# Optimization experiments

Measured on AMD Instinct MI355X. Metric: run time of the kernel, lower is better.

The kernel has to match this reference:

```python
import jax, jax.numpy as jnp
import numpy as np

N_NODES = 50000
N_EDGES = 800000
D = 64  # in_dim = hidden = out_dim
LEAKY_SLOPE = 0.01  # F.leaky_relu default


def gat_layer(h, src, dst, W, b, aW, ab):
    # fc: z = h @ W.T + b            [N, D_out]
    z = h @ W.T + b
    zs = z[src]                       # gather src feats  [E, D_out]
    zd = z[dst]                       # gather dst feats  [E, D_out]
    # attn_fc(concat(z_src, z_dst)) -> scalar per edge, then leaky_relu
    e = jnp.concatenate([zs, zd], axis=-1) @ aW.T + ab   # [E, 1]
    e = jax.nn.leaky_relu(e, LEAKY_SLOPE)[:, 0]          # [E]
    # softmax over incoming edges per destination node (mailbox softmax)
    m = jax.ops.segment_max(e, dst, num_segments=N_NODES)    # [N]
    ex = jnp.exp(e - m[dst])
    den = jax.ops.segment_sum(ex, dst, num_segments=N_NODES)  # [N]
    alpha = ex / den[dst]                                      # [E]
    # scatter-sum aggregate of alpha * z_src
    return jax.ops.segment_sum(alpha[:, None] * zs, dst, num_segments=N_NODES)


def setup_inputs() -> dict:
    key = jax.random.key(0)
    ks = jax.random.split(key, 16)
    x = jax.random.normal(ks[0], (N_NODES, D), dtype=jnp.float32)
    src = jax.random.randint(ks[1], (N_EDGES,), 0, N_NODES)
    dst = jax.random.randint(ks[2], (N_EDGES,), 0, N_NODES)
    # xavier_normal with relu gain, per reset_parameters
    gain = float(np.sqrt(2.0))
    params = {}
    for i in range(3):
        std_fc = gain * np.sqrt(2.0 / (D + D))
        std_at = gain * np.sqrt(2.0 / (2 * D + 1))
        params[f"W{i}"] = jax.random.normal(ks[3 + 4 * i], (D, D), dtype=jnp.float32) * std_fc
        params[f"b{i}"] = jnp.zeros((D,), dtype=jnp.float32)
        params[f"a{i}"] = jax.random.normal(ks[4 + 4 * i], (1, 2 * D), dtype=jnp.float32) * std_at
        params[f"ab{i}"] = jnp.zeros((1,), dtype=jnp.float32)
    return {"x": x, "src": src, "dst": dst, **params}


def reference(x, src, dst, W0, b0, a0, ab0, W1, b1, a1, ab1, W2, b2, a2, ab2):
    h = gat_layer(x, src, dst, W0, b0, a0, ab0)
    h = jax.nn.relu(h)
    h = gat_layer(h, src, dst, W1, b1, a1, ab1)
    h = jax.nn.relu(h)
    h = gat_layer(h, src, dst, W2, b2, a2, ab2)
    return h
```

## Files before the change

### kernel.cpp

```cpp
#include <hip/hip_runtime.h>
#include <math.h>

#define N_NODES 50000
#define N_EDGES 800000
#define D 64

#define NB 256
#define NBLK 256
#define BUCKET_NODES 196
#define TILE 3125

typedef unsigned short ushort_t;

__device__ __forceinline__ ushort_t f32_to_bf16(float f) {
    unsigned u = __float_as_uint(f);
    u += 0x7fffu + ((u >> 16) & 1u);
    return (ushort_t)(u >> 16);
}

template<int N>
__global__ void scan_partial_g(const int* __restrict__ in, int* __restrict__ partials) {
    const int base = blockIdx.x * 1024 + threadIdx.x * 4;
    int4 c = make_int4(0, 0, 0, 0);
    if (base + 3 < N) c = *(const int4*)&in[base];
    else { int* cp = (int*)&c; for (int j = 0; j < 4; ++j) if (base + j < N) cp[j] = in[base + j]; }
    int s = c.x + c.y + c.z + c.w;
    #pragma unroll
    for (int off = 32; off >= 1; off >>= 1) s += __shfl_xor(s, off, 64);
    __shared__ int red[4];
    if ((threadIdx.x & 63) == 0) red[threadIdx.x >> 6] = s;
    __syncthreads();
    if (threadIdx.x == 0) partials[blockIdx.x] = red[0] + red[1] + red[2] + red[3];
}

template<int N, int NT>
__global__ void scan_write_i(const int* __restrict__ in, const int* __restrict__ partials_raw,
                             int* __restrict__ out) {
    __shared__ int toff;
    __shared__ int sh[256];
    const int tid = threadIdx.x;
    if (tid < 64) {
        const int v = (tid < NT) ? partials_raw[tid] : 0;
        int inc = v;
        #pragma unroll
        for (int off = 1; off < 64; off <<= 1) {
            const int w = __shfl_up(inc, off, 64);
            if (tid >= off) inc += w;
        }
        if (tid == blockIdx.x) toff = inc - v;
    }
    const int base = blockIdx.x * 1024 + tid * 4;
    int4 c = make_int4(0, 0, 0, 0);
    if (base + 3 < N) c = *(const int4*)&in[base];
    else { int* cp = (int*)&c; for (int j = 0; j < 4; ++j) if (base + j < N) cp[j] = in[base + j]; }
    const int s = c.x + c.y + c.z + c.w;
    sh[tid] = s;
    __syncthreads();
    for (int off = 1; off < 256; off <<= 1) {
        const int w = (tid >= off) ? sh[tid - off] : 0;
        __syncthreads();
        sh[tid] += w;
        __syncthreads();
    }
    int run = toff + sh[tid] - s;
    const int* cp = (const int*)&c;
    int rp[4];
    #pragma unroll
    for (int j = 0; j < 4; ++j) { rp[j] = run; run += cp[j]; }
    if (base + 3 < N) *(int4*)&out[base] = make_int4(rp[0], rp[1], rp[2], rp[3]);
    else for (int j = 0; j < 4; ++j) if (base + j < N) out[base + j] = rp[j];
}

__global__ __launch_bounds__(256) void bucket_hist(const int* __restrict__ dst,
                                                   int* __restrict__ Acnt) {
    __shared__ int hist[NB];
    for (int i = threadIdx.x; i < NB; i += 256) hist[i] = 0;
    __syncthreads();
    const int base = blockIdx.x * TILE;
    for (int i = threadIdx.x; i < TILE; i += 256)
        atomicAdd(&hist[dst[base + i] / BUCKET_NODES], 1);
    __syncthreads();
    for (int bk = threadIdx.x; bk < NB; bk += 256)
        Acnt[bk * NBLK + blockIdx.x] = hist[bk];
}

__global__ __launch_bounds__(256) void bucket_scatter(const int* __restrict__ src,
                                                      const int* __restrict__ dst,
                                                      const int* __restrict__ offs,
                                                      int2* __restrict__ staging) {
    __shared__ int cur[NB];
    for (int i = threadIdx.x; i < NB; i += 256) cur[i] = offs[i * NBLK + blockIdx.x];
    __syncthreads();
    const int base = blockIdx.x * TILE;
    for (int i = threadIdx.x; i < TILE; i += 256) {
        const int s = src[base + i], d = dst[base + i];
        const int pos = atomicAdd(&cur[d / BUCKET_NODES], 1);
        staging[pos] = make_int2(s, d);
    }
}

__global__ __launch_bounds__(256) void node_counts(const int2* __restrict__ staging,
                                                   const int* __restrict__ offs,
                                                   int* __restrict__ counts,
                                                   int* __restrict__ bucket_sum) {
    __shared__ int cnt[BUCKET_NODES];
    __shared__ int red[4];
    const int b = blockIdx.x, tid = threadIdx.x;
    for (int i = tid; i < BUCKET_NODES; i += 256) cnt[i] = 0;
    __syncthreads();
    const int s0 = offs[b * NBLK];
    const int s1 = (b == NB - 1) ? N_EDGES : offs[(b + 1) * NBLK];
    for (int i = s0 + tid; i < s1; i += 256)
        atomicAdd(&cnt[staging[i].y - b * BUCKET_NODES], 1);
    __syncthreads();
    for (int i = tid; i < BUCKET_NODES; i += 256) {
        const int node = b * BUCKET_NODES + i;
        if (node < N_NODES) counts[node] = cnt[i];
    }
    int s = (tid < BUCKET_NODES) ? cnt[tid] : 0;
    #pragma unroll
    for (int off = 32; off >= 1; off >>= 1) s += __shfl_xor(s, off, 64);
    if ((tid & 63) == 0) red[tid >> 6] = s;
    __syncthreads();
    if (tid == 0) bucket_sum[b] = red[0] + red[1] + red[2] + red[3];
}

__global__ __launch_bounds__(256) void row_ptr_build(const int* __restrict__ counts,
                                                     const int* __restrict__ bucket_sum,
                                                     int* __restrict__ row_ptr) {
    __shared__ int bs[NB];
    __shared__ int loc[256];
    const int b = blockIdx.x, tid = threadIdx.x;
    bs[tid] = bucket_sum[tid];
    __syncthreads();
    for (int off = 1; off < 256; off <<= 1) {
        const int w = (tid >= off) ? bs[tid - off] : 0;
        __syncthreads();
        bs[tid] += w;
        __syncthreads();
    }
    const int bucket_off = bs[b] - bucket_sum[b];
    const int node = b * BUCKET_NODES + tid;
    const int c = (tid < BUCKET_NODES && node < N_NODES) ? counts[node] : 0;
    loc[tid] = c;
    __syncthreads();
    for (int off = 1; off < 256; off <<= 1) {
        const int w = (tid >= off) ? loc[tid - off] : 0;
        __syncthreads();
        loc[tid] += w;
        __syncthreads();
    }
    if (tid < BUCKET_NODES && node < N_NODES) row_ptr[node] = bucket_off + loc[tid] - c;
    if (b == 0 && tid == 0) row_ptr[N_NODES] = N_EDGES;
}

__global__ __launch_bounds__(256) void bucket_to_csr(const int2* __restrict__ staging,
                                                     const int* __restrict__ offs,
                                                     const int* __restrict__ row_ptr,
                                                     int* __restrict__ csr_src) {
    __shared__ int cur[BUCKET_NODES];
    const int b = blockIdx.x;
    for (int i = threadIdx.x; i < BUCKET_NODES; i += 256) {
        const int node = b * BUCKET_NODES + i;
        cur[i] = (node < N_NODES) ? row_ptr[node] : 0;
    }
    __syncthreads();
    const int s0 = offs[b * NBLK];
    const int s1 = (b == NB - 1) ? N_EDGES : offs[(b + 1) * NBLK];
    for (int i = s0 + threadIdx.x; i < s1; i += 256) {
        const int2 e = staging[i];
        const int pos = atomicAdd(&cur[e.y - b * BUCKET_NODES], 1);
        csr_src[pos] = e.x;
    }
}

#define NL_ROWS 8
__global__ __launch_bounds__(256) void node_linear_gemm(
    const float* __restrict__ h, ushort_t* __restrict__ zb,
    const float* __restrict__ W, const float* __restrict__ b,
    const float* __restrict__ a, const float* __restrict__ ab,
    float* __restrict__ s_src, float* __restrict__ s_dst)
{
    __shared__ float Wt[64 * 65];
    for (int idx = threadIdx.x; idx < D * D; idx += 256) {
        const int j = idx >> 6, k = idx & 63;
        Wt[k * 65 + j] = W[idx];
    }
    __syncthreads();

    const int lane = threadIdx.x & 63;
    const int wv   = __builtin_amdgcn_readfirstlane(threadIdx.x >> 6);
    const int row0 = (blockIdx.x * 4 + wv) * NL_ROWS;
    if (row0 >= N_NODES) return;

    const float bj  = b[lane];
    const float alo = a[lane];
    const float ahi = a[64 + lane];

    const float* hr[NL_ROWS];
    #pragma unroll
    for (int r = 0; r < NL_ROWS; ++r) hr[r] = h + (size_t)(row0 + r) * D;

    float acc[NL_ROWS];
    #pragma unroll
    for (int r = 0; r < NL_ROWS; ++r) acc[r] = bj;

    #pragma unroll 4
    for (int k = 0; k < D; ++k) {
        const float wkj = Wt[k * 65 + lane];
        #pragma unroll
        for (int r = 0; r < NL_ROWS; ++r)
            acc[r] = fmaf(hr[r][k], wkj, acc[r]);
    }

    #pragma unroll
    for (int r = 0; r < NL_ROWS; ++r) {
        zb[(size_t)(row0 + r) * D + lane] = f32_to_bf16(acc[r]);
        float u = acc[r] * alo;
        float v = acc[r] * ahi;
        #pragma unroll
        for (int off = 32; off >= 1; off >>= 1) {
            u += __shfl_xor(u, off, 64);
            v += __shfl_xor(v, off, 64);
        }
        if (lane == 0) { s_src[row0 + r] = u; s_dst[row0 + r] = v + ab[0]; }
    }
}

template<bool RELU>
__global__ __launch_bounds__(256) void fused_softmax_gather(
    const int* __restrict__ row_ptr, const int* __restrict__ csr_src,
    const float* __restrict__ s_src, const float* __restrict__ s_dst,
    const ushort_t* __restrict__ zb, float* __restrict__ out)
{
    __shared__ int2 sh[4][64];
    const int lane = threadIdx.x & 63;
    const int wv   = threadIdx.x >> 6;
    const int g    = lane >> 4;
    const int sl   = lane & 15;
    const int node0 = (blockIdx.x * 4 + wv) * 4;
    if (node0 >= N_NODES) return;
    const int mynode = node0 + g;

    const int beg = row_ptr[mynode];
    const int end = row_ptr[mynode + 1];
    const float sd = s_dst[mynode];
    float m = -INFINITY, den = 0.f;
    for (int base = beg; base < end; base += 16) {
        const int n = min(16, end - base);
        float e = -INFINITY;
        if (sl < n) {
            const int s = csr_src[base + sl];
            e = s_src[s] + sd;
            e = e > 0.f ? e : 0.01f * e;
        }
        float mc = e;
        #pragma unroll
        for (int off = 8; off >= 1; off >>= 1) mc = fmaxf(mc, __shfl_xor(mc, off, 64));
        if (mc > m) { den *= __expf(m - mc); m = mc; }
        float ex = (sl < n) ? __expf(e - m) : 0.f;
        #pragma unroll
        for (int off = 8; off >= 1; off >>= 1) ex += __shfl_xor(ex, off, 64);
        den += ex;
    }
    const float invden = (den > 0.f) ? 1.f / den : 0.f;

    const int half = lane >> 5;
    const int fl   = lane & 31;
    #pragma unroll
    for (int q = 0; q < 4; ++q) {
        const int nq    = node0 + q;
        const int begq  = __shfl(beg, q * 16, 64);
        const int endq  = __shfl(end, q * 16, 64);
        const float mq  = __shfl(m, q * 16, 64);
        const float ivq = __shfl(invden, q * 16, 64);
        const float sdq = __shfl(sd, q * 16, 64);

        float2 acc[8];
        #pragma unroll
        for (int p = 0; p < 8; ++p) acc[p] = make_float2(0.f, 0.f);

        for (int base = begq; base < endq; base += 64) {
            const int n = min(64, endq - base);
            int2 ws = make_int2(0, 0);
            if (lane < n) {
                const int s = csr_src[base + lane];
                float e = s_src[s] + sdq;
                e = e > 0.f ? e : 0.01f * e;
                ws = make_int2(__float_as_int(__expf(e - mq) * ivq), s);
            }
            sh[wv][lane] = ws;
            for (int t = 0; t < n; t += 16) {
                #pragma unroll
                for (int p = 0; p < 8; ++p) {
                    const int ei = t + 2 * p + half;
                    const int2 w2 = sh[wv][ei];
                    const float w = __int_as_float(w2.x);
                    const unsigned u = *(const unsigned*)&zb[(size_t)w2.y * D + 2 * fl];
                    acc[p].x = fmaf(w, __uint_as_float(u << 16), acc[p].x);
                    acc[p].y = fmaf(w, __uint_as_float(u & 0xffff0000u), acc[p].y);
                }
            }
        }
        float2 tot = make_float2(0.f, 0.f);
        #pragma unroll
        for (int p = 0; p < 8; ++p) { tot.x += acc[p].x; tot.y += acc[p].y; }
        tot.x += __shfl_xor(tot.x, 32, 64);
        tot.y += __shfl_xor(tot.y, 32, 64);
        if (RELU) { tot.x = fmaxf(tot.x, 0.f); tot.y = fmaxf(tot.y, 0.f); }
        if (half == 0)
            *(float2*)&out[(size_t)nq * D + 2 * fl] = tot;
    }
}

extern "C" void kernel_launch(void* const* d_in, const int* in_sizes, int n_in,
                              void* d_out, int out_size, void* d_ws, size_t ws_size,
                              hipStream_t stream) {
    const float* x   = (const float*)d_in[0];
    const int*   src = (const int*)d_in[1];
    const int*   dst = (const int*)d_in[2];
    float* out = (float*)d_out;

    char* wp = (char*)d_ws;
    auto alloc = [&](size_t bytes) -> void* {
        void* p = (void*)wp;
        wp += (bytes + 255) & ~(size_t)255;
        return p;
    };
    ushort_t* zb      = (ushort_t*)alloc((size_t)N_NODES * D * sizeof(ushort_t));
    float* s_src      = (float*)alloc((size_t)N_NODES * sizeof(float));
    float* s_dst      = (float*)alloc((size_t)N_NODES * sizeof(float));
    int*   counts     = (int*)alloc((size_t)N_NODES * sizeof(int));
    int*   row_ptr    = (int*)alloc((size_t)(N_NODES + 1) * sizeof(int));
    int*   csr_src    = (int*)alloc((size_t)N_EDGES * sizeof(int));
    int*   partB      = (int*)alloc(64 * sizeof(int));
    int*   bucket_sum = (int*)alloc((size_t)NB * sizeof(int));
    int*   Acnt       = (int*)alloc((size_t)NB * NBLK * sizeof(int));
    int*   offs       = (int*)alloc((size_t)NB * NBLK * sizeof(int));
    int2*  staging    = (int2*)alloc((size_t)N_EDGES * sizeof(int2));
    (void)ws_size;

    bucket_hist<<<NBLK, 256, 0, stream>>>(dst, Acnt);
    scan_partial_g<NB * NBLK><<<64, 256, 0, stream>>>(Acnt, partB);
    scan_write_i<NB * NBLK, 64><<<64, 256, 0, stream>>>(Acnt, partB, offs);
    bucket_scatter<<<NBLK, 256, 0, stream>>>(src, dst, offs, staging);
    node_counts<<<NB, 256, 0, stream>>>(staging, offs, counts, bucket_sum);
    row_ptr_build<<<NB, 256, 0, stream>>>(counts, bucket_sum, row_ptr);
    bucket_to_csr<<<NB, 256, 0, stream>>>(staging, offs, row_ptr, csr_src);

    const int grid_k1 = (N_NODES + 4 * NL_ROWS - 1) / (4 * NL_ROWS);
    const int grid_fg = N_NODES / 16;

    for (int layer = 0; layer < 3; ++layer) {
        const float* W  = (const float*)d_in[3 + 4 * layer];
        const float* b  = (const float*)d_in[4 + 4 * layer];
        const float* a  = (const float*)d_in[5 + 4 * layer];
        const float* ab = (const float*)d_in[6 + 4 * layer];
        const float* hin = (layer == 0) ? x : out;

        node_linear_gemm<<<grid_k1, 256, 0, stream>>>(hin, zb, W, b, a, ab, s_src, s_dst);
        if (layer < 2) {
            fused_softmax_gather<true ><<<grid_fg, 256, 0, stream>>>(row_ptr, csr_src, s_src, s_dst, zb, out);
        } else {
            fused_softmax_gather<false><<<grid_fg, 256, 0, stream>>>(row_ptr, csr_src, s_src, s_dst, zb, out);
        }
    }
}
```

Baseline: 199.6 us.

## Interleave gather of four destination nodes per wave in one edge loop

The aggregation phase now handles the four nodes owned by a wave together instead of one after another. Edge weights for all four nodes are staged in shared memory, then a single loop walks up to the largest degree and issues gathers for all four nodes in each step. The aim is more independent memory loads in flight and fewer serialized short loops. The cost is padded work: the loop runs to the maximum of the four degrees, and zero-weighted rows get loaded where a node has fewer edges.

```diff
diff --git a/kernel.cpp b/kernel.cpp
--- a/kernel.cpp
+++ b/kernel.cpp
@@ -233,7 +233,7 @@
     const float* __restrict__ s_src, const float* __restrict__ s_dst,
     const ushort_t* __restrict__ zb, float* __restrict__ out)
 {
-    __shared__ int2 sh[4][64];
+    __shared__ int2 sh[4][4][64];
     const int lane = threadIdx.x & 63;
     const int wv   = threadIdx.x >> 6;
     const int g    = lane >> 4;
@@ -265,51 +265,68 @@
     }
     const float invden = (den > 0.f) ? 1.f / den : 0.f;
 
+    int begq[4], endq[4];
+    float mq[4], ivq[4], sdq[4];
+    #pragma unroll
+    for (int q = 0; q < 4; ++q) {
+        begq[q] = __shfl(beg, q * 16, 64);
+        endq[q] = __shfl(end, q * 16, 64);
+        mq[q]   = __shfl(m, q * 16, 64);
+        ivq[q]  = __shfl(invden, q * 16, 64);
+        sdq[q]  = __shfl(sd, q * 16, 64);
+    }
+    int maxdeg = 0;
+    #pragma unroll
+    for (int q = 0; q < 4; ++q) maxdeg = max(maxdeg, endq[q] - begq[q]);
+
     const int half = lane >> 5;
     const int fl   = lane & 31;
+    float2 acc[4][2];
     #pragma unroll
     for (int q = 0; q < 4; ++q) {
-        const int nq    = node0 + q;
-        const int begq  = __shfl(beg, q * 16, 64);
-        const int endq  = __shfl(end, q * 16, 64);
-        const float mq  = __shfl(m, q * 16, 64);
-        const float ivq = __shfl(invden, q * 16, 64);
-        const float sdq = __shfl(sd, q * 16, 64);
-
-        float2 acc[8];
-        #pragma unroll
-        for (int p = 0; p < 8; ++p) acc[p] = make_float2(0.f, 0.f);
-
-        for (int base = begq; base < endq; base += 64) {
-            const int n = min(64, endq - base);
+        acc[q][0] = make_float2(0.f, 0.f);
+        acc[q][1] = make_float2(0.f, 0.f);
+    }
+
+    for (int c = 0; c < maxdeg; c += 64) {
+        #pragma unroll
+        for (int q = 0; q < 4; ++q) {
             int2 ws = make_int2(0, 0);
-            if (lane < n) {
-                const int s = csr_src[base + lane];
-                float e = s_src[s] + sdq;
+            const int i = begq[q] + c + lane;
+            if (i < endq[q]) {
+                const int s = csr_src[i];
+                float e = s_src[s] + sdq[q];
                 e = e > 0.f ? e : 0.01f * e;
-                ws = make_int2(__float_as_int(__expf(e - mq) * ivq), s);
+                ws = make_int2(__float_as_int(__expf(e - mq[q]) * ivq[q]), s);
             }
-            sh[wv][lane] = ws;
-            for (int t = 0; t < n; t += 16) {
-                #pragma unroll
-                for (int p = 0; p < 8; ++p) {
-                    const int ei = t + 2 * p + half;
-                    const int2 w2 = sh[wv][ei];
-                    const float w = __int_as_float(w2.x);
-                    const unsigned u = *(const unsigned*)&zb[(size_t)w2.y * D + 2 * fl];
-                    acc[p].x = fmaf(w, __uint_as_float(u << 16), acc[p].x);
-                    acc[p].y = fmaf(w, __uint_as_float(u & 0xffff0000u), acc[p].y);
-                }
+            sh[wv][q][lane] = ws;
+        }
+        const int n = min(64, maxdeg - c);
+        for (int t = 0; t < n; t += 4) {
+            #pragma unroll
+            for (int q = 0; q < 4; ++q) {
+                const int2 wa = sh[wv][q][t + half];
+                const int2 wb = sh[wv][q][t + 2 + half];
+                const unsigned ua = *(const unsigned*)&zb[(size_t)wa.y * D + 2 * fl];
+                const unsigned ub = *(const unsigned*)&zb[(size_t)wb.y * D + 2 * fl];
+                const float fa = __int_as_float(wa.x);
+                const float fb = __int_as_float(wb.x);
+                acc[q][0].x = fmaf(fa, __uint_as_float(ua << 16), acc[q][0].x);
+                acc[q][0].y = fmaf(fa, __uint_as_float(ua & 0xffff0000u), acc[q][0].y);
+                acc[q][1].x = fmaf(fb, __uint_as_float(ub << 16), acc[q][1].x);
+                acc[q][1].y = fmaf(fb, __uint_as_float(ub & 0xffff0000u), acc[q][1].y);
             }
         }
-        float2 tot = make_float2(0.f, 0.f);
-        #pragma unroll
-        for (int p = 0; p < 8; ++p) { tot.x += acc[p].x; tot.y += acc[p].y; }
+    }
+    #pragma unroll
+    for (int q = 0; q < 4; ++q) {
+        float2 tot = make_float2(acc[q][0].x + acc[q][1].x,
+                                 acc[q][0].y + acc[q][1].y);
         tot.x += __shfl_xor(tot.x, 32, 64);
         tot.y += __shfl_xor(tot.y, 32, 64);
         if (RELU) { tot.x = fmaxf(tot.x, 0.f); tot.y = fmaxf(tot.y, 0.f); }
         if (half == 0)
-            *(float2*)&out[(size_t)nq * D + 2 * fl] = tot;
+            *(float2*)&out[(size_t)(node0 + q) * D + 2 * fl] = tot;
     }
 }
 
```

New measurement: 197.5 us, median of 2. Within noise of the previous version (-1.0%).
